# Performance work log

Hardware: AMD Instinct MI355X
Metric: run time of the kernel (lower is better)

Reference implementation:

```python
import jax, jax.numpy as jnp
import numpy as np

N = 8192
NHID = 256

def setup_inputs() -> dict:
    key = jax.random.key(0)
    ks = jax.random.split(key, 9)
    s = 1.0 / np.sqrt(NHID)  # torch Linear default init scale
    return {
        "x1": jax.random.normal(ks[0], (N, NHID), jnp.float32),
        "x2": jax.random.normal(ks[1], (N, NHID), jnp.float32),
        "x3": jax.random.normal(ks[2], (N, NHID), jnp.float32),
        "Wq": jax.random.uniform(ks[3], (NHID, NHID), jnp.float32, -s, s),
        "bq": jax.random.uniform(ks[4], (NHID,), jnp.float32, -s, s),
        "Wk": jax.random.uniform(ks[5], (NHID, NHID), jnp.float32, -s, s),
        "bk": jax.random.uniform(ks[6], (NHID,), jnp.float32, -s, s),
        "Wv": jax.random.uniform(ks[7], (NHID, NHID), jnp.float32, -s, s),
        "bv": jax.random.uniform(ks[8], (NHID,), jnp.float32, -s, s),
    }

def reference(x1, x2, x3, Wq, bq, Wk, bk, Wv, bv):
    # torch.nn.Linear: y = x @ W.T + b
    q = x1 @ Wq.T + bq                      # [N, nhid]
    k = x2 @ Wk.T + bk                      # [N, nhid]
    v = x3 @ Wv.T + bv                      # [N, nhid]
    scores = q @ k.T                        # [N, N], NOTE: unscaled (no 1/sqrt(d))
    attn = jax.nn.softmax(scores, axis=1)   # softmax over keys (dim=1)
    return attn @ v                         # [N, nhid]
```

## Files before the change

### kernel.cpp

```cpp
#include <hip/hip_runtime.h>
#include <stdint.h>

typedef unsigned short u16;
typedef __attribute__((ext_vector_type(8))) short short8;
typedef __attribute__((ext_vector_type(4))) float f32x4;
typedef __attribute__((ext_vector_type(16))) float f32x16;

#define LOG2E 1.4426950408889634f
#define NT 8192
#define DH 256

#define QH     0
#define KH     2097152
#define VTB    4194304
#define OPARTB 6291456
#define XH0 6291456
#define XL0 8388608
#define XH1 10485760
#define XL1 12582912
#define XH2 14680064
#define XL2 16777216
#define WQH 18874368
#define WQL 18939904
#define WKH 19005440
#define WKL 19070976
#define WVH 19136512
#define WVL 19202048
#define MPART_F 11534336
#define LPART_F 11599872

__device__ __forceinline__ u16 f2bf(float f) {
  union { float f; uint32_t u; } c; c.f = f;
  uint32_t u = c.u;
  return (u16)((u + 0x7fffu + ((u >> 16) & 1)) >> 16);
}
__device__ __forceinline__ float bf2f(u16 h) {
  union { uint32_t u; float f; } c; c.u = ((uint32_t)h) << 16;
  return c.f;
}

__device__ __forceinline__ int swz32(int u, int h) {
  return (u & 24) | ((u & 7) ^ (h & 7));
}

__device__ __forceinline__ f32x4 mfma16(short8 a, short8 b, f32x4 c) {
  return __builtin_amdgcn_mfma_f32_16x16x32_bf16(a, b, c, 0, 0, 0);
}
__device__ __forceinline__ f32x16 mfma32(short8 a, short8 b, f32x16 c) {
  return __builtin_amdgcn_mfma_f32_32x32x16_bf16(a, b, c, 0, 0, 0);
}

__device__ __forceinline__ void gl_lds16(const u16* g, u16* l) {
  __builtin_amdgcn_global_load_lds(
      (const __attribute__((address_space(1))) uint32_t*)g,
      (__attribute__((address_space(3))) uint32_t*)l, 16, 0, 0);
}

__global__ __launch_bounds__(256) void k_convert(
    const float* __restrict__ x1, const float* __restrict__ x2, const float* __restrict__ x3,
    const float* __restrict__ wq, const float* __restrict__ wk, const float* __restrict__ wv,
    u16* __restrict__ wsu) {
  int b = blockIdx.x;
  const float* src; u16 *dh, *dl; int bl;
  if (b < 1024)      { src = x1; dh = wsu + XH0; dl = wsu + XL0; bl = b; }
  else if (b < 2048) { src = x2; dh = wsu + XH1; dl = wsu + XL1; bl = b - 1024; }
  else if (b < 3072) { src = x3; dh = wsu + XH2; dl = wsu + XL2; bl = b - 2048; }
  else if (b < 3104) { src = wq; dh = wsu + WQH; dl = wsu + WQL; bl = b - 3072; }
  else if (b < 3136) { src = wk; dh = wsu + WKH; dl = wsu + WKL; bl = b - 3104; }
  else               { src = wv; dh = wsu + WVH; dl = wsu + WVL; bl = b - 3136; }
  int i = (bl * 256 + threadIdx.x) * 8;
  f32x4 a = *(const f32x4*)(src + i);
  f32x4 c = *(const f32x4*)(src + i + 4);
  short8 rh, rl;
  float v[8] = {a[0], a[1], a[2], a[3], c[0], c[1], c[2], c[3]};
#pragma unroll
  for (int j = 0; j < 8; j++) {
    u16 h = f2bf(v[j]);
    rh[j] = (short)h;
    rl[j] = (short)f2bf(v[j] - bf2f(h));
  }
  *(short8*)(dh + i) = rh;
  *(short8*)(dl + i) = rl;
}

__global__ __launch_bounds__(256) void k_qkv(
    u16* __restrict__ wsu,
    const float* __restrict__ bq, const float* __restrict__ bk, const float* __restrict__ bv) {
  __shared__ u16 sAh[32 * 256];
  __shared__ u16 sAl[32 * 256];
  __shared__ u16 sBh[32 * 256];
  __shared__ u16 sBl[32 * 256];
  int bx = blockIdx.x;
  int mid = bx >> 8;
  int t = bx & 255;
  const u16 *Ah, *Al, *Bh, *Bl; u16 *O; const float* bias;
  int rowA0, colBase, ldO, biasRow;
  if (mid == 0) {
    Ah = wsu + XH0; Al = wsu + XL0; Bh = wsu + WQH; Bl = wsu + WQL;
    O = wsu + QH; bias = bq; biasRow = 0; ldO = 256;
    rowA0 = t * 32; colBase = 0;
  } else if (mid == 1) {
    Ah = wsu + XH1; Al = wsu + XL1; Bh = wsu + WKH; Bl = wsu + WKL;
    O = wsu + KH; bias = bk; biasRow = 0; ldO = 256;
    rowA0 = t * 32; colBase = 0;
  } else {
    Ah = wsu + WVH; Al = wsu + WVL; Bh = wsu + XH2; Bl = wsu + XL2;
    O = wsu + VTB; bias = bv; biasRow = 1; ldO = 8192;
    rowA0 = (t & 7) * 32; colBase = (t >> 3) * 256;
  }

  int tid = threadIdx.x;
  int lane = tid & 63, wave = tid >> 6;
  int n = lane & 15, quad = lane >> 4;
  int wm = wave >> 1, wn = wave & 1;

#pragma unroll
  for (int i = 0; i < 4; i++) {
    int L = i * 256 + tid;
    int row = L >> 5, u = L & 31;
    short8 vh = *(const short8*)(Ah + (size_t)(rowA0 + row) * 256 + u * 8);
    short8 vl = *(const short8*)(Al + (size_t)(rowA0 + row) * 256 + u * 8);
    *(short8*)(&sAh[row * 256 + swz32(u, row) * 8]) = vh;
    *(short8*)(&sAl[row * 256 + swz32(u, row) * 8]) = vl;
  }

  int brow0 = wave * 2 + (lane >> 5);
  int bgu = (lane & 24) | ((lane & 7) ^ (brow0 & 7));

#pragma unroll
  for (int i = 0; i < 4; i++) {
    gl_lds16(Bh + (size_t)(colBase + i * 8 + brow0) * 256 + bgu * 8, &sBh[i * 2048 + wave * 512]);
    gl_lds16(Bl + (size_t)(colBase + i * 8 + brow0) * 256 + bgu * 8, &sBl[i * 2048 + wave * 512]);
  }

#pragma unroll 1
  for (int g = 0; g < 8; g++) {
    __syncthreads();

    int colg = colBase + g * 32 + wn * 16 + n;
    f32x4 acc = {0.f, 0.f, 0.f, 0.f};
#pragma unroll
    for (int kk = 0; kk < 8; kk++) {
      int ra = wm * 16 + n;
      int rbB = wn * 16 + n;
      short8 ah = *(const short8*)(&sAh[ra * 256 + swz32(kk * 4 + quad, ra) * 8]);
      short8 al = *(const short8*)(&sAl[ra * 256 + swz32(kk * 4 + quad, ra) * 8]);
      short8 bh = *(const short8*)(&sBh[rbB * 256 + swz32(kk * 4 + quad, rbB) * 8]);
      short8 bl = *(const short8*)(&sBl[rbB * 256 + swz32(kk * 4 + quad, rbB) * 8]);
      acc = mfma16(ah, bh, acc);
      acc = mfma16(ah, bl, acc);
      acc = mfma16(al, bh, acc);
    }

    if (g < 7) {
      __syncthreads();
      int b0 = colBase + (g + 1) * 32;
#pragma unroll
      for (int i = 0; i < 4; i++) {
        gl_lds16(Bh + (size_t)(b0 + i * 8 + brow0) * 256 + bgu * 8, &sBh[i * 2048 + wave * 512]);
        gl_lds16(Bl + (size_t)(b0 + i * 8 + brow0) * 256 + bgu * 8, &sBl[i * 2048 + wave * 512]);
      }
    }

    float bcol = biasRow ? 0.0f : bias[colg];
#pragma unroll
    for (int r = 0; r < 4; r++) {
      int rowg = rowA0 + wm * 16 + quad * 4 + r;
      float bb = biasRow ? bias[rowg] : bcol;
      O[(size_t)rowg * ldO + colg] = f2bf(acc[r] + bb);
    }
  }
}

__global__ __launch_bounds__(256, 2) void k_flash(
    const u16* __restrict__ wsu, u16* __restrict__ opart, float* __restrict__ wsf) {
  __shared__ u16 smem[32768];

  int qb = blockIdx.x >> 3, sp = blockIdx.x & 7;
  int tid = threadIdx.x, lane = tid & 63, wave = tid >> 6;
  int key = lane & 31;
  int h = lane >> 5;
  const u16* Qp = wsu + QH;
  const u16* Kp = wsu + KH;
  const u16* Vp = wsu + VTB;

  int rowQ0 = qb * 128 + wave * 32;

  short8 qf[16];
#pragma unroll
  for (int kk = 0; kk < 16; kk++)
    qf[kk] = *(const short8*)(Qp + (size_t)(rowQ0 + key) * 256 + kk * 16 + h * 8);

  int koff[4];
#pragma unroll
  for (int m = 0; m < 4; m++)
    koff[m] = key * 512 + 16 * ((2 * m + h) ^ (key & 7));
  int voff[2];
#pragma unroll
  for (int c = 0; c < 2; c++)
    voff[c] = key * 64 + 16 * ((2 * c + h) ^ ((key >> 1) & 3));

  int krow0 = wave * 2 + h;
  int kgu = (lane & 24) | ((lane & 7) ^ (krow0 & 7));
  int vd_base = wave * 16 + (lane >> 2);
  int vgu = (lane & 3) ^ ((lane >> 3) & 3);

  int key00 = sp * 1024;

#pragma unroll
  for (int i = 0; i < 4; i++) {
    gl_lds16(Kp + (size_t)(key00 + i * 8 + krow0) * 256 + kgu * 8,
             &smem[i * 2048 + wave * 512]);
    gl_lds16(Vp + (size_t)(i * 64 + vd_base) * 8192 + key00 + vgu * 8,
             &smem[16384 + i * 2048 + wave * 512]);
  }

  f32x16 o[8];
#pragma unroll
  for (int dt = 0; dt < 8; dt++)
#pragma unroll
    for (int r = 0; r < 16; r++) o[dt][r] = 0.f;
  float negm0 = 0.f, lcur = 0.f;

#pragma unroll 1
  for (int it = 0; it < 32; it++) {
    __syncthreads();
    int cur = it & 1;
    const u16* sKc = &smem[cur * 8192];
    const u16* sVc = &smem[16384 + cur * 8192];
    if (it + 1 < 32) {
      int k1 = key00 + (it + 1) * 32;
      int nb = cur ^ 1;
#pragma unroll
      for (int i = 0; i < 4; i++) {
        gl_lds16(Kp + (size_t)(k1 + i * 8 + krow0) * 256 + kgu * 8,
                 &smem[nb * 8192 + i * 2048 + wave * 512]);
        gl_lds16(Vp + (size_t)(i * 64 + vd_base) * 8192 + k1 + vgu * 8,
                 &smem[16384 + nb * 8192 + i * 2048 + wave * 512]);
      }
    }

    f32x16 s;
#pragma unroll
    for (int r = 0; r < 16; r++) s[r] = 0.f;
    __builtin_amdgcn_s_setprio(1);
#pragma unroll
    for (int kk = 0; kk < 16; kk++) {
      short8 kf = *(const short8*)((const char*)sKc + koff[kk & 3] + 128 * (kk >> 2));
      s = mfma32(kf, qf[kk], s);
    }
    __builtin_amdgcn_s_setprio(0);

    if (it == 0) {
      float mv = s[0];
#pragma unroll
      for (int r = 1; r < 16; r++) mv = fmaxf(mv, s[r]);
      mv = fmaxf(mv, __shfl_xor(mv, 32));
      negm0 = -mv * LOG2E;
    }

    uint32_t c8[8];
#pragma unroll
    for (int j = 0; j < 8; j++) {
      float x0 = fminf(fmaf(s[2 * j],     LOG2E, negm0), 110.f);
      float x1 = fminf(fmaf(s[2 * j + 1], LOG2E, negm0), 110.f);
      float p0 = exp2f(x0);
      float p1 = exp2f(x1);
      lcur += p0 + p1;
      asm("v_cvt_pk_bf16_f32 %0, %1, %2" : "=v"(c8[j]) : "v"(p0), "v"(p1));
    }
    uint32_t w0a = c8[0], w2a = c8[2], w1a = c8[1], w3a = c8[3];
    asm("v_permlane32_swap_b32 %0, %1" : "+v"(w0a), "+v"(w2a));
    asm("v_permlane32_swap_b32 %0, %1" : "+v"(w1a), "+v"(w3a));
    uint32_t w0b = c8[4], w2b = c8[6], w1b = c8[5], w3b = c8[7];
    asm("v_permlane32_swap_b32 %0, %1" : "+v"(w0b), "+v"(w2b));
    asm("v_permlane32_swap_b32 %0, %1" : "+v"(w1b), "+v"(w3b));
    union { uint32_t u[4]; short8 s8; } pb0, pb1;
    pb0.u[0] = w0a; pb0.u[1] = w1a; pb0.u[2] = w2a; pb0.u[3] = w3a;
    pb1.u[0] = w0b; pb1.u[1] = w1b; pb1.u[2] = w2b; pb1.u[3] = w3b;

    __builtin_amdgcn_s_setprio(1);
#pragma unroll
    for (int dt = 0; dt < 8; dt++) {
      short8 v0 = *(const short8*)((const char*)sVc + voff[0] + dt * 2048);
      o[dt] = mfma32(v0, pb0.s8, o[dt]);
    }
#pragma unroll
    for (int dt = 0; dt < 8; dt++) {
      short8 v1 = *(const short8*)((const char*)sVc + voff[1] + dt * 2048);
      o[dt] = mfma32(v1, pb1.s8, o[dt]);
    }
    __builtin_amdgcn_s_setprio(0);
  }

  lcur += __shfl_xor(lcur, 32);

  __syncthreads();
  u16* tb = &smem[wave * 8192];
#pragma unroll
  for (int dt = 0; dt < 8; dt++)
#pragma unroll
    for (int j = 0; j < 4; j++) {
      uint32_t a, b;
      asm("v_cvt_pk_bf16_f32 %0, %1, %2" : "=v"(a) : "v"(o[dt][4 * j + 0]), "v"(o[dt][4 * j + 1]));
      asm("v_cvt_pk_bf16_f32 %0, %1, %2" : "=v"(b) : "v"(o[dt][4 * j + 2]), "v"(o[dt][4 * j + 3]));
      int u16i = (dt * 4 + j) ^ (key & 7);
      uint2 val; val.x = a; val.y = b;
      *(uint2*)((char*)tb + key * 512 + u16i * 16 + h * 8) = val;
    }
  u16* op = opart + (size_t)sp * (NT * DH);
#pragma unroll
  for (int c2i = 0; c2i < 16; c2i++) {
    int rl = c2i * 2 + h;
    int uu = lane & 31;
    short8 vv = *(const short8*)((const char*)tb + rl * 512 + ((uu ^ (rl & 7)) * 16));
    *(short8*)(op + (size_t)(rowQ0 + rl) * 256 + uu * 8) = vv;
  }

  if (lane < 32) {
    int row = rowQ0 + key;
    wsf[MPART_F + sp * NT + row] = negm0 * -0.6931471805599453f;
    wsf[LPART_F + sp * NT + row] = lcur;
  }
}

__global__ __launch_bounds__(256) void k_combine(
    const u16* __restrict__ opart, const float* __restrict__ wsf, float* __restrict__ out) {
  int gid = blockIdx.x * 256 + threadIdx.x;
  int row = gid >> 6, cg = gid & 63;
  float m[8], l[8];
#pragma unroll
  for (int s = 0; s < 8; s++) {
    m[s] = wsf[MPART_F + s * NT + row];
    l[s] = wsf[LPART_F + s * NT + row];
  }
  float ms = m[0];
#pragma unroll
  for (int s = 1; s < 8; s++) ms = fmaxf(ms, m[s]);
  float denom = 0.f;
  float acc[4] = {0.f, 0.f, 0.f, 0.f};
#pragma unroll
  for (int s = 0; s < 8; s++) {
    float w = exp2f((m[s] - ms) * LOG2E);
    denom += w * l[s];
    const u16* pp = opart + ((size_t)s * NT + row) * 256 + cg * 4;
    uint2 v = *(const uint2*)pp;
    acc[0] += w * bf2f((u16)(v.x & 0xffff));
    acc[1] += w * bf2f((u16)(v.x >> 16));
    acc[2] += w * bf2f((u16)(v.y & 0xffff));
    acc[3] += w * bf2f((u16)(v.y >> 16));
  }
  float inv = 1.0f / denom;
  f32x4 r = {acc[0] * inv, acc[1] * inv, acc[2] * inv, acc[3] * inv};
  *(f32x4*)(out + (size_t)row * 256 + cg * 4) = r;
}

extern "C" void kernel_launch(void* const* d_in, const int* in_sizes, int n_in,
                              void* d_out, int out_size, void* d_ws, size_t ws_size,
                              hipStream_t stream) {
  const float* x1 = (const float*)d_in[0];
  const float* x2 = (const float*)d_in[1];
  const float* x3 = (const float*)d_in[2];
  const float* Wq = (const float*)d_in[3];
  const float* bq = (const float*)d_in[4];
  const float* Wk = (const float*)d_in[5];
  const float* bk = (const float*)d_in[6];
  const float* Wv = (const float*)d_in[7];
  const float* bv = (const float*)d_in[8];
  u16* wsu = (u16*)d_ws;
  float* wsf = (float*)d_ws;
  float* out = (float*)d_out;

  k_convert<<<dim3(3168), dim3(256), 0, stream>>>(x1, x2, x3, Wq, Wk, Wv, wsu);
  k_qkv<<<dim3(768), dim3(256), 0, stream>>>(wsu, bq, bk, bv);
  k_flash<<<dim3(512), dim3(256), 0, stream>>>(wsu, wsu + OPARTB, wsf);
  k_combine<<<dim3(2048), dim3(256), 0, stream>>>(wsu + OPARTB, wsf, out);
}
```

Baseline: 205.8 us.

## Software-pipeline PV MFMA one iteration behind QK to overlap softmax

Restructures the attention loop so the P·V MFMAs for the previous key block are issued right after the current block's Q·K MFMAs, then softmax runs. The PV product is delayed one iteration and a tail step is added after the loop. V loads are now issued for the current block, not prefetched a block ahead. The goal is to let exp/convert/permlane VALU work overlap with matrix-core work instead of serialising. This costs extra live registers for the carried P fragments, and V loads get less lead time before use.

```diff
diff --git a/kernel.cpp b/kernel.cpp
--- a/kernel.cpp
+++ b/kernel.cpp
@@ -211,8 +211,6 @@
   for (int i = 0; i < 4; i++) {
     gl_lds16(Kp + (size_t)(key00 + i * 8 + krow0) * 256 + kgu * 8,
              &smem[i * 2048 + wave * 512]);
-    gl_lds16(Vp + (size_t)(i * 64 + vd_base) * 8192 + key00 + vgu * 8,
-             &smem[16384 + i * 2048 + wave * 512]);
   }
 
   f32x16 o[8];
@@ -221,24 +219,33 @@
 #pragma unroll
     for (int r = 0; r < 16; r++) o[dt][r] = 0.f;
   float negm0 = 0.f, lcur = 0.f;
+
+  union PB { uint32_t u[4]; short8 s8; };
+  PB pb0, pb1;
+#pragma unroll
+  for (int j = 0; j < 4; j++) { pb0.u[j] = 0u; pb1.u[j] = 0u; }
 
 #pragma unroll 1
   for (int it = 0; it < 32; it++) {
     __syncthreads();
     int cur = it & 1;
     const u16* sKc = &smem[cur * 8192];
-    const u16* sVc = &smem[16384 + cur * 8192];
     if (it + 1 < 32) {
       int k1 = key00 + (it + 1) * 32;
-      int nb = cur ^ 1;
-#pragma unroll
-      for (int i = 0; i < 4; i++) {
+#pragma unroll
+      for (int i = 0; i < 4; i++)
         gl_lds16(Kp + (size_t)(k1 + i * 8 + krow0) * 256 + kgu * 8,
-                 &smem[nb * 8192 + i * 2048 + wave * 512]);
-        gl_lds16(Vp + (size_t)(i * 64 + vd_base) * 8192 + k1 + vgu * 8,
-                 &smem[16384 + nb * 8192 + i * 2048 + wave * 512]);
-      }
-    }
+                 &smem[(cur ^ 1) * 8192 + i * 2048 + wave * 512]);
+    }
+    {
+      int kv = key00 + it * 32;
+#pragma unroll
+      for (int i = 0; i < 4; i++)
+        gl_lds16(Vp + (size_t)(i * 64 + vd_base) * 8192 + kv + vgu * 8,
+                 &smem[16384 + cur * 8192 + i * 2048 + wave * 512]);
+    }
+
+    const u16* sVp = (it > 0) ? &smem[16384 + (cur ^ 1) * 8192] : sKc;
 
     f32x16 s;
 #pragma unroll
@@ -248,6 +255,16 @@
     for (int kk = 0; kk < 16; kk++) {
       short8 kf = *(const short8*)((const char*)sKc + koff[kk & 3] + 128 * (kk >> 2));
       s = mfma32(kf, qf[kk], s);
+    }
+#pragma unroll
+    for (int dt = 0; dt < 8; dt++) {
+      short8 v0 = *(const short8*)((const char*)sVp + voff[0] + dt * 2048);
+      o[dt] = mfma32(v0, pb0.s8, o[dt]);
+    }
+#pragma unroll
+    for (int dt = 0; dt < 8; dt++) {
+      short8 v1 = *(const short8*)((const char*)sVp + voff[1] + dt * 2048);
+      o[dt] = mfma32(v1, pb1.s8, o[dt]);
     }
     __builtin_amdgcn_s_setprio(0);
 
@@ -275,19 +292,22 @@
     uint32_t w0b = c8[4], w2b = c8[6], w1b = c8[5], w3b = c8[7];
     asm("v_permlane32_swap_b32 %0, %1" : "+v"(w0b), "+v"(w2b));
     asm("v_permlane32_swap_b32 %0, %1" : "+v"(w1b), "+v"(w3b));
-    union { uint32_t u[4]; short8 s8; } pb0, pb1;
     pb0.u[0] = w0a; pb0.u[1] = w1a; pb0.u[2] = w2a; pb0.u[3] = w3a;
     pb1.u[0] = w0b; pb1.u[1] = w1b; pb1.u[2] = w2b; pb1.u[3] = w3b;
-
+  }
+
+  __syncthreads();
+  {
+    const u16* sVp = &smem[16384 + 8192];
     __builtin_amdgcn_s_setprio(1);
 #pragma unroll
     for (int dt = 0; dt < 8; dt++) {
-      short8 v0 = *(const short8*)((const char*)sVc + voff[0] + dt * 2048);
+      short8 v0 = *(const short8*)((const char*)sVp + voff[0] + dt * 2048);
       o[dt] = mfma32(v0, pb0.s8, o[dt]);
     }
 #pragma unroll
     for (int dt = 0; dt < 8; dt++) {
-      short8 v1 = *(const short8*)((const char*)sVc + voff[1] + dt * 2048);
+      short8 v1 = *(const short8*)((const char*)sVp + voff[1] + dt * 2048);
       o[dt] = mfma32(v1, pb1.s8, o[dt]);
     }
     __builtin_amdgcn_s_setprio(0);
```

New measurement: 207.1 us. No clear change (+0.6%).
